# Kernel optimization log

Hardware: AMD Instinct MI355X
Metric: run time of the kernel (lower is better)

## Reference

```python
import jax, jax.numpy as jnp
import numpy as np

N_USER = 50000
N_ITEM = 50000
N_EDGE = 600000
D = 128


def _mean_agg(msg, dst, num_nodes):
    # segment-sum of messages and edge counts; nodes with no in-edges get 0 (DGL semantics)
    s = jax.ops.segment_sum(msg, dst, num_segments=num_nodes)
    cnt = jax.ops.segment_sum(jnp.ones((dst.shape[0], 1), msg.dtype), dst, num_segments=num_nodes)
    return s / jnp.maximum(cnt, 1.0)


def setup_inputs() -> dict:
    key = jax.random.key(0)
    ks = jax.random.split(key, 14)
    scale = 1.0 / np.sqrt(D)
    return {
        "feat_user": jax.random.normal(ks[0], (N_USER, D), jnp.float32),
        "feat_item": jax.random.normal(ks[1], (N_ITEM, D), jnp.float32),
        "W_uu": jax.random.normal(ks[2], (D, D), jnp.float32) * scale,
        "b_uu": jax.random.normal(ks[3], (D,), jnp.float32) * scale,
        "W_ub": jax.random.normal(ks[4], (D, D), jnp.float32) * scale,
        "b_ub": jax.random.normal(ks[5], (D,), jnp.float32) * scale,
        "W_iu": jax.random.normal(ks[6], (D, D), jnp.float32) * scale,
        "b_iu": jax.random.normal(ks[7], (D,), jnp.float32) * scale,
        "src_uu": jax.random.randint(ks[8], (N_EDGE,), 0, N_USER, jnp.int32),
        "dst_uu": jax.random.randint(ks[9], (N_EDGE,), 0, N_USER, jnp.int32),
        "src_ub": jax.random.randint(ks[10], (N_EDGE,), 0, N_USER, jnp.int32),
        "dst_ub": jax.random.randint(ks[11], (N_EDGE,), 0, N_ITEM, jnp.int32),
        "src_iu": jax.random.randint(ks[12], (N_EDGE,), 0, N_ITEM, jnp.int32),
        "dst_iu": jax.random.randint(ks[13], (N_EDGE,), 0, N_USER, jnp.int32),
    }


def reference(feat_user, feat_item, W_uu, b_uu, W_ub, b_ub, W_iu, b_iu,
              src_uu, dst_uu, src_ub, dst_ub, src_iu, dst_iu):
    # per-edge-type linear projection of src node features
    Wh_uu = feat_user @ W_uu + b_uu   # (user, follows, user)
    Wh_ub = feat_user @ W_ub + b_ub   # (user, buys, item)
    Wh_iu = feat_item @ W_iu + b_iu   # (item, bought_by, user)
    # copy_u -> mean per dst node, per edge type
    h_uu = _mean_agg(Wh_uu[src_uu], dst_uu, N_USER)
    h_ub = _mean_agg(Wh_ub[src_ub], dst_ub, N_ITEM)
    h_iu = _mean_agg(Wh_iu[src_iu], dst_iu, N_USER)
    # cross-type combine = 'sum' per dst ntype
    out_user = h_uu + h_iu
    out_item = h_ub
    return out_user, out_item
```

## Files before the change

kernel.cpp:

```cpp
#include <hip/hip_runtime.h>
#include <stdint.h>
#include <string.h>

#define N_USER 50000
#define N_ITEM 50000
#define N_EDGE 600000
#define D 128
#define NTOT 150000
#define ETOT 1800000
#define NB 147
#define BSH 10
#define SPAN 1024
#define CHUNK 4096

typedef unsigned short u16;
typedef unsigned int   u32;
typedef __attribute__((ext_vector_type(8))) short short8;
typedef __attribute__((ext_vector_type(4))) float floatx4;

static __device__ __forceinline__ u16 f2b(float f) {
  u32 x; memcpy(&x, &f, 4);
  u32 r = x + 0x7fffu + ((x >> 16) & 1u);
  return (u16)(r >> 16);
}
static __device__ __forceinline__ float blo2f(u32 v) {
  u32 x = v << 16; float f; memcpy(&f, &x, 4); return f;
}
static __device__ __forceinline__ float bhi2f(u32 v) {
  u32 x = v & 0xffff0000u; float f; memcpy(&f, &x, 4); return f;
}

__global__ void __launch_bounds__(256) k_front(
    const int* __restrict__ duu, const int* __restrict__ dub, const int* __restrict__ diu,
    int* __restrict__ bhist,
    const float* __restrict__ W0, const float* __restrict__ W1, const float* __restrict__ W2,
    u16* __restrict__ WT,
    const float* __restrict__ fu, const float* __restrict__ fi,
    u16* __restrict__ fb_u, u16* __restrict__ fb_i) {
  int bid = blockIdx.x;
  if (bid < 440) {
    __shared__ int h[NB];
    for (int i = threadIdx.x; i < NB; i += 256) h[i] = 0;
    __syncthreads();
    int base = bid * CHUNK;
    for (int j = threadIdx.x; j < CHUNK; j += 256) {
      int e = base + j;
      if (e < ETOT) {
        int t = e / N_EDGE, i = e - t * N_EDGE;
        int d = (t == 0) ? duu[i] : ((t == 1) ? dub[i] : diu[i]);
        atomicAdd(&h[(t * N_USER + d) >> BSH], 1);
      }
    }
    __syncthreads();
    for (int i = threadIdx.x; i < NB; i += 256) if (h[i]) atomicAdd(&bhist[i], h[i]);
  } else if (bid < 443) {
    int wsel = bid - 440;
    for (int idx = threadIdx.x; idx < D * D; idx += 256) {
      int n = idx >> 7, k = idx & 127;
      if (wsel == 0)      WT[n * 256 + k]       = f2b(W0[k * D + n]);
      else if (wsel == 1) WT[n * 256 + 128 + k] = f2b(W2[k * D + n]);
      else                WT[32768 + n * D + k] = f2b(W1[k * D + n]);
    }
  } else {
    int g = bid - 443;
    const float* src = fu; u16* dst = fb_u;
    if (g >= 6250) { g -= 6250; src = fi; dst = fb_i; }
    int gid = g * 256 + threadIdx.x;
    float4 v = ((const float4*)src)[gid];
    union { u16 u[4]; uint2 d; } pk;
    pk.u[0] = f2b(v.x); pk.u[1] = f2b(v.y); pk.u[2] = f2b(v.z); pk.u[3] = f2b(v.w);
    ((uint2*)dst)[gid] = pk.d;
  }
}

__global__ void __launch_bounds__(256) k_bplace(
    const int* __restrict__ suu, const int* __restrict__ duu,
    const int* __restrict__ sub, const int* __restrict__ dub,
    const int* __restrict__ siu, const int* __restrict__ diu,
    const int* __restrict__ bhist, int* __restrict__ cursor,
    int* __restrict__ boff, u32* __restrict__ ebuf) {
  __shared__ int h[NB];
  __shared__ int sboff[NB];
  __shared__ int buf[256];
  int t = threadIdx.x;
  int v = (t < NB) ? bhist[t] : 0;
  buf[t] = v; __syncthreads();
  for (int s = 1; s < 256; s <<= 1) {
    int y = (t >= s) ? buf[t - s] : 0;
    __syncthreads(); buf[t] += y; __syncthreads();
  }
  if (t < NB) sboff[t] = (t == 0) ? 0 : buf[t - 1];
  if (blockIdx.x == 0 && t <= NB) boff[t] = (t == 0) ? 0 : buf[t - 1];
  for (int i = t; i < NB; i += 256) h[i] = 0;
  __syncthreads();
  int base = blockIdx.x * CHUNK;
  u32 pay[16], br[16];
#pragma unroll
  for (int k = 0; k < 16; ++k) {
    int e = base + k * 256 + t;
    br[k] = 0xFFFFFFFFu;
    if (e < ETOT) {
      int ty = e / N_EDGE, i = e - ty * N_EDGE;
      int d, s;
      if (ty == 0)      { d = duu[i]; s = suu[i]; }
      else if (ty == 1) { d = dub[i]; s = sub[i]; }
      else              { d = diu[i]; s = siu[i]; }
      int slot = ty * N_USER + d;
      int bu = slot >> BSH;
      int rank = atomicAdd(&h[bu], 1);
      pay[k] = (u32)s | ((u32)(slot & (SPAN - 1)) << 16);
      br[k]  = (u32)bu | ((u32)rank << 8);
    }
  }
  __syncthreads();
  for (int i = t; i < NB; i += 256)
    h[i] = sboff[i] + atomicAdd(&cursor[i], h[i]);
  __syncthreads();
#pragma unroll
  for (int k = 0; k < 16; ++k) {
    if (br[k] != 0xFFFFFFFFu) {
      int bu = br[k] & 0xFF, rank = (int)(br[k] >> 8);
      ebuf[h[bu] + rank] = pay[k];
    }
  }
}

__global__ void __launch_bounds__(256) k_csr(const int* __restrict__ boff, const u32* __restrict__ ebuf,
                                             int* __restrict__ off, u16* __restrict__ ssrc) {
  __shared__ int sc[SPAN];
  __shared__ int so[SPAN];
  __shared__ int part[256];
  int b = blockIdx.x;
  int ebase = boff[b], ecnt = boff[b + 1] - ebase;
  int sbase = b << BSH;
  int nslots = (NTOT - sbase < SPAN) ? (NTOT - sbase) : SPAN;
  for (int i = threadIdx.x; i < SPAN; i += 256) sc[i] = 0;
  __syncthreads();
  for (int j = threadIdx.x; j < ecnt; j += 256)
    atomicAdd(&sc[ebuf[ebase + j] >> 16], 1);
  __syncthreads();
  int t = threadIdx.x;
  int s0 = sc[4*t], s1 = sc[4*t+1], s2 = sc[4*t+2], s3 = sc[4*t+3];
  int tsum = s0 + s1 + s2 + s3;
  part[t] = tsum; __syncthreads();
  for (int s = 1; s < 256; s <<= 1) {
    int y = (t >= s) ? part[t - s] : 0;
    __syncthreads(); part[t] += y; __syncthreads();
  }
  int pbase = part[t] - tsum;
  so[4*t]   = pbase;
  so[4*t+1] = pbase + s0;
  so[4*t+2] = pbase + s0 + s1;
  so[4*t+3] = pbase + s0 + s1 + s2;
  __syncthreads();
  for (int i = threadIdx.x; i < nslots; i += 256)
    off[sbase + i] = ebase + so[i];
  if (b == 0 && threadIdx.x == 0) off[NTOT] = ETOT;
  for (int i = threadIdx.x; i < SPAN; i += 256) sc[i] = so[i];
  __syncthreads();
  for (int j = threadIdx.x; j < ecnt; j += 256) {
    u32 p = ebuf[ebase + j];
    int pos = atomicAdd(&sc[p >> 16], 1);
    ssrc[ebase + pos] = (u16)(p & 0xFFFFu);
  }
}

__global__ void __launch_bounds__(256) k_mean(const u16* __restrict__ fb_u, const u16* __restrict__ fb_i,
                                              const int* __restrict__ off, const u16* __restrict__ ssrc,
                                              u16* __restrict__ ob) {
  int slot = blockIdx.x * 8 + (threadIdx.x >> 5);
  int lane = threadIdx.x & 31;
  if (slot >= NTOT) return;
  int t = slot / N_USER;
  int d = slot - t * N_USER;
  const u16* fb = (t == 2) ? fb_i : fb_u;
  int s = off[slot], e = off[slot + 1];
  int n = e - s;
  int my_src = (lane < n) ? (int)ssrc[s + lane] : 0;
  float a0 = 0.f, a1 = 0.f, a2 = 0.f, a3 = 0.f;
  int m = (n < 32) ? n : 32;
  int i = 0;
  for (; i + 4 <= m; i += 4) {
    int s0 = __shfl(my_src, i, 32);
    int s1 = __shfl(my_src, i + 1, 32);
    int s2 = __shfl(my_src, i + 2, 32);
    int s3 = __shfl(my_src, i + 3, 32);
    uint2 v0 = ((const uint2*)(fb + (size_t)s0 * D))[lane];
    uint2 v1 = ((const uint2*)(fb + (size_t)s1 * D))[lane];
    uint2 v2 = ((const uint2*)(fb + (size_t)s2 * D))[lane];
    uint2 v3 = ((const uint2*)(fb + (size_t)s3 * D))[lane];
    a0 += blo2f(v0.x) + blo2f(v1.x) + blo2f(v2.x) + blo2f(v3.x);
    a1 += bhi2f(v0.x) + bhi2f(v1.x) + bhi2f(v2.x) + bhi2f(v3.x);
    a2 += blo2f(v0.y) + blo2f(v1.y) + blo2f(v2.y) + blo2f(v3.y);
    a3 += bhi2f(v0.y) + bhi2f(v1.y) + bhi2f(v2.y) + bhi2f(v3.y);
  }
  for (; i < m; ++i) {
    int sr = __shfl(my_src, i, 32);
    uint2 v = ((const uint2*)(fb + (size_t)sr * D))[lane];
    a0 += blo2f(v.x); a1 += bhi2f(v.x);
    a2 += blo2f(v.y); a3 += bhi2f(v.y);
  }
  for (int j = s + 32; j < e; ++j) {
    int sr = ssrc[j];
    uint2 v = ((const uint2*)(fb + (size_t)sr * D))[lane];
    a0 += blo2f(v.x); a1 += bhi2f(v.x);
    a2 += blo2f(v.y); a3 += bhi2f(v.y);
  }
  float inv = (n > 0) ? 1.0f / (float)n : 0.f;
  u32 p0 = (u32)f2b(a0 * inv) | ((u32)f2b(a1 * inv) << 16);
  u32 p1 = (u32)f2b(a2 * inv) | ((u32)f2b(a3 * inv) << 16);
  u32* mrow;
  if (t == 0)      mrow = (u32*)(ob + (size_t)d * 256);
  else if (t == 2) mrow = (u32*)(ob + (size_t)d * 256 + 128);
  else             mrow = (u32*)(ob + 12800000 + (size_t)d * 256);
  ((uint2*)mrow)[lane] = make_uint2(p0, p1);
}

__global__ void __launch_bounds__(256, 2) k_out(float* out, const u16* __restrict__ WT,
                                                const float* __restrict__ buu, const float* __restrict__ bub,
                                                const float* __restrict__ biu, const int* __restrict__ off) {
  int users = (blockIdx.y == 0);
  int tid = threadIdx.x;
  int w = tid >> 6, lane = tid & 63, quad = lane >> 4, l16 = lane & 15;
  int KT = users ? 8 : 4;
  const u16* Wsrc = users ? WT : (WT + 32768);
  int wstride = users ? 256 : 128;

  __shared__ u16 sB[32768];
  int nfrag = KT * 8 * 64;
  for (int fid = tid; fid < nfrag; fid += 256) {
    int fl = fid & 63, fnt = (fid >> 6) & 7, fkk = fid >> 9;
    int fq = fl >> 4, fl16 = fl & 15;
    const u16* src = Wsrc + (fnt * 16 + fl16) * wstride + fkk * 32 + fq * 8;
    *(uint4*)(sB + (size_t)fid * 8) = *(const uint4*)src;
  }
  __syncthreads();

  int row0 = blockIdx.x * 128 + w * 32;
  const u16* ob = (const u16*)out;
  const u16* Abase = users ? ob : (ob + 12800000);
  size_t outoff = users ? 0 : (size_t)N_USER;

  int r0a = row0 + l16, r1a = row0 + 16 + l16;
  int rA0 = r0a < N_USER ? r0a : N_USER - 1;
  int rA1 = r1a < N_USER ? r1a : N_USER - 1;
  const u16* A0 = Abase + (size_t)rA0 * 256 + quad * 8;
  const u16* A1 = Abase + (size_t)rA1 * 256 + quad * 8;

  floatx4 acc[2][8];
#pragma unroll
  for (int rt = 0; rt < 2; ++rt)
#pragma unroll
    for (int nt = 0; nt < 8; ++nt) acc[rt][nt] = (floatx4){0.f, 0.f, 0.f, 0.f};

  for (int kk = 0; kk < KT; ++kk) {
    short8 af0 = *(const short8*)(A0 + kk * 32);
    short8 af1 = *(const short8*)(A1 + kk * 32);
    const short8* bp = (const short8*)(sB + ((size_t)kk * 8 * 64 + lane) * 8);
#pragma unroll
    for (int nt = 0; nt < 8; ++nt) {
      short8 bf = bp[nt * 64];
      acc[0][nt] = __builtin_amdgcn_mfma_f32_16x16x32_bf16(af0, bf, acc[0][nt], 0, 0, 0);
      acc[1][nt] = __builtin_amdgcn_mfma_f32_16x16x32_bf16(af1, bf, acc[1][nt], 0, 0, 0);
    }
  }

#pragma unroll
  for (int rt = 0; rt < 2; ++rt) {
    int tbase = row0 + rt * 16;
    int nA[4], nB[4];
#pragma unroll
    for (int i = 0; i < 4; ++i) {
      int grow = tbase + quad * 4 + i;
      bool ok = grow < N_USER;
      if (users) {
        nA[i] = ok ? (off[grow + 1] - off[grow]) : 0;
        nB[i] = ok ? (off[2 * N_USER + grow + 1] - off[2 * N_USER + grow]) : 0;
      } else {
        nA[i] = ok ? (off[N_USER + grow + 1] - off[N_USER + grow]) : 0;
        nB[i] = 0;
      }
    }
#pragma unroll
    for (int nt = 0; nt < 8; ++nt) {
      int col = nt * 16 + l16;
      float bA = users ? buu[col] : bub[col];
      float bB = users ? biu[col] : 0.f;
#pragma unroll
      for (int i = 0; i < 4; ++i) {
        int grow = tbase + quad * 4 + i;
        if (grow < N_USER) {
          float r = acc[rt][nt][i] + (nA[i] > 0 ? bA : 0.f) + (nB[i] > 0 ? bB : 0.f);
          out[(outoff + (size_t)grow) * D + col] = r;
        }
      }
    }
  }
}

extern "C" void kernel_launch(void* const* d_in, const int* in_sizes, int n_in,
                              void* d_out, int out_size, void* d_ws, size_t ws_size,
                              hipStream_t stream) {
  const float* fu  = (const float*)d_in[0];
  const float* fi  = (const float*)d_in[1];
  const float* Wuu = (const float*)d_in[2];
  const float* buu = (const float*)d_in[3];
  const float* Wub = (const float*)d_in[4];
  const float* bub = (const float*)d_in[5];
  const float* Wiu = (const float*)d_in[6];
  const float* biu = (const float*)d_in[7];
  const int* suu = (const int*)d_in[8];
  const int* duu = (const int*)d_in[9];
  const int* sub = (const int*)d_in[10];
  const int* dub = (const int*)d_in[11];
  const int* siu = (const int*)d_in[12];
  const int* diu = (const int*)d_in[13];
  float* out = (float*)d_out;
  u16* ob = (u16*)d_out;

  int* wsi    = (int*)d_ws;
  int* off    = wsi;
  int* bhist  = wsi + 150016;
  int* cursor = wsi + 150208;
  int* boff   = wsi + 150400;
  u32* ebuf   = (u32*)(wsi + 150592);
  u16* ssrc   = (u16*)(wsi + 1950592);
  u16* WT     = (u16*)(wsi + 2850592);
  u16* fb_u   = (u16*)(wsi + 2875168);
  u16* fb_i   = (u16*)(wsi + 6075168);

  hipMemsetAsync(bhist, 0, 384 * sizeof(int), stream);
  k_front<<<443 + 12500, 256, 0, stream>>>(duu, dub, diu, bhist, Wuu, Wub, Wiu, WT,
                                           fu, fi, fb_u, fb_i);
  k_bplace<<<440, 256, 0, stream>>>(suu, duu, sub, dub, siu, diu, bhist, cursor, boff, ebuf);
  k_csr<<<NB, 256, 0, stream>>>(boff, ebuf, off, ssrc);
  k_mean<<<18750, 256, 0, stream>>>(fb_u, fb_i, off, ssrc, ob);
  k_out<<<dim3(391, 2), 256, 0, stream>>>(out, WT, buu, bub, biu, off);
}
```

Measured before the change: 286.4 us.

## Halve CSR bucket span, batch bf16 conversion per block, prefetch GEMM operands

The destination bucket size drops from 1024 to 512 slots, doubling the bucket count so the CSR-building kernel runs more blocks with less work each. The scans and rank packing are adjusted to handle two buckets per thread and 9-bit bucket ids. The feature-to-bf16 conversion now does eight float4 per thread in fewer blocks instead of one each. In the output GEMM, all A fragments and the degree counts are loaded before the shared-memory barrier so global latency overlaps the weight staging, at the cost of more registers.

New measurement: 279.9 us. -2.3%, faster.

```diff
diff --git a/kernel.cpp b/kernel.cpp
--- a/kernel.cpp
+++ b/kernel.cpp
@@ -8,9 +8,9 @@
 #define D 128
 #define NTOT 150000
 #define ETOT 1800000
-#define NB 147
-#define BSH 10
-#define SPAN 1024
+#define NB 293
+#define BSH 9
+#define SPAN 512
 #define CHUNK 4096
 
 typedef unsigned short u16;
@@ -62,14 +62,19 @@
       else                WT[32768 + n * D + k] = f2b(W1[k * D + n]);
     }
   } else {
-    int g = bid - 443;
-    const float* src = fu; u16* dst = fb_u;
-    if (g >= 6250) { g -= 6250; src = fi; dst = fb_i; }
-    int gid = g * 256 + threadIdx.x;
-    float4 v = ((const float4*)src)[gid];
-    union { u16 u[4]; uint2 d; } pk;
-    pk.u[0] = f2b(v.x); pk.u[1] = f2b(v.y); pk.u[2] = f2b(v.z); pk.u[3] = f2b(v.w);
-    ((uint2*)dst)[gid] = pk.d;
+    int base = (bid - 443) * 2048;
+#pragma unroll
+    for (int u = 0; u < 8; ++u) {
+      int gid = base + u * 256 + threadIdx.x;
+      if (gid < 3200000) {
+        const float* src = fu; u16* dst = fb_u; int g = gid;
+        if (g >= 1600000) { g -= 1600000; src = fi; dst = fb_i; }
+        float4 v = ((const float4*)src)[g];
+        union { u16 u[4]; uint2 d; } pk;
+        pk.u[0] = f2b(v.x); pk.u[1] = f2b(v.y); pk.u[2] = f2b(v.z); pk.u[3] = f2b(v.w);
+        ((uint2*)dst)[g] = pk.d;
+      }
+    }
   }
 }
 
@@ -83,14 +88,21 @@
   __shared__ int sboff[NB];
   __shared__ int buf[256];
   int t = threadIdx.x;
-  int v = (t < NB) ? bhist[t] : 0;
-  buf[t] = v; __syncthreads();
+  int a = (2 * t < NB) ? bhist[2 * t] : 0;
+  int b = (2 * t + 1 < NB) ? bhist[2 * t + 1] : 0;
+  buf[t] = a + b; __syncthreads();
   for (int s = 1; s < 256; s <<= 1) {
     int y = (t >= s) ? buf[t - s] : 0;
     __syncthreads(); buf[t] += y; __syncthreads();
   }
-  if (t < NB) sboff[t] = (t == 0) ? 0 : buf[t - 1];
-  if (blockIdx.x == 0 && t <= NB) boff[t] = (t == 0) ? 0 : buf[t - 1];
+  int ex = buf[t] - (a + b);
+  if (2 * t < NB) sboff[2 * t] = ex;
+  if (2 * t + 1 < NB) sboff[2 * t + 1] = ex + a;
+  if (blockIdx.x == 0) {
+    if (2 * t < NB) boff[2 * t] = ex;
+    if (2 * t + 1 < NB) boff[2 * t + 1] = ex + a;
+    if (t == 255) boff[NB] = buf[255];
+  }
   for (int i = t; i < NB; i += 256) h[i] = 0;
   __syncthreads();
   int base = blockIdx.x * CHUNK;
@@ -109,7 +121,7 @@
       int bu = slot >> BSH;
       int rank = atomicAdd(&h[bu], 1);
       pay[k] = (u32)s | ((u32)(slot & (SPAN - 1)) << 16);
-      br[k]  = (u32)bu | ((u32)rank << 8);
+      br[k]  = (u32)bu | ((u32)rank << 9);
     }
   }
   __syncthreads();
@@ -119,7 +131,7 @@
 #pragma unroll
   for (int k = 0; k < 16; ++k) {
     if (br[k] != 0xFFFFFFFFu) {
-      int bu = br[k] & 0xFF, rank = (int)(br[k] >> 8);
+      int bu = br[k] & 0x1FF, rank = (int)(br[k] >> 9);
       ebuf[h[bu] + rank] = pay[k];
     }
   }
@@ -140,18 +152,16 @@
     atomicAdd(&sc[ebuf[ebase + j] >> 16], 1);
   __syncthreads();
   int t = threadIdx.x;
-  int s0 = sc[4*t], s1 = sc[4*t+1], s2 = sc[4*t+2], s3 = sc[4*t+3];
-  int tsum = s0 + s1 + s2 + s3;
+  int s0 = sc[2 * t], s1 = sc[2 * t + 1];
+  int tsum = s0 + s1;
   part[t] = tsum; __syncthreads();
   for (int s = 1; s < 256; s <<= 1) {
     int y = (t >= s) ? part[t - s] : 0;
     __syncthreads(); part[t] += y; __syncthreads();
   }
   int pbase = part[t] - tsum;
-  so[4*t]   = pbase;
-  so[4*t+1] = pbase + s0;
-  so[4*t+2] = pbase + s0 + s1;
-  so[4*t+3] = pbase + s0 + s1 + s2;
+  so[2 * t]     = pbase;
+  so[2 * t + 1] = pbase + s0;
   __syncthreads();
   for (int i = threadIdx.x; i < nslots; i += 256)
     off[sbase + i] = ebase + so[i];
@@ -234,7 +244,6 @@
     const u16* src = Wsrc + (fnt * 16 + fl16) * wstride + fkk * 32 + fq * 8;
     *(uint4*)(sB + (size_t)fid * 8) = *(const uint4*)src;
   }
-  __syncthreads();
 
   int row0 = blockIdx.x * 128 + w * 32;
   const u16* ob = (const u16*)out;
@@ -247,40 +256,53 @@
   const u16* A0 = Abase + (size_t)rA0 * 256 + quad * 8;
   const u16* A1 = Abase + (size_t)rA1 * 256 + quad * 8;
 
+  short8 af0[8], af1[8];
+#pragma unroll
+  for (int kk = 0; kk < 8; ++kk) {
+    if (kk < KT) {
+      af0[kk] = *(const short8*)(A0 + kk * 32);
+      af1[kk] = *(const short8*)(A1 + kk * 32);
+    }
+  }
+  int nA[2][4], nB[2][4];
+#pragma unroll
+  for (int rt = 0; rt < 2; ++rt)
+#pragma unroll
+    for (int i = 0; i < 4; ++i) {
+      int grow = row0 + rt * 16 + quad * 4 + i;
+      bool ok = grow < N_USER;
+      if (users) {
+        nA[rt][i] = ok ? (off[grow + 1] - off[grow]) : 0;
+        nB[rt][i] = ok ? (off[2 * N_USER + grow + 1] - off[2 * N_USER + grow]) : 0;
+      } else {
+        nA[rt][i] = ok ? (off[N_USER + grow + 1] - off[N_USER + grow]) : 0;
+        nB[rt][i] = 0;
+      }
+    }
+  __syncthreads();
+
   floatx4 acc[2][8];
 #pragma unroll
   for (int rt = 0; rt < 2; ++rt)
 #pragma unroll
     for (int nt = 0; nt < 8; ++nt) acc[rt][nt] = (floatx4){0.f, 0.f, 0.f, 0.f};
 
-  for (int kk = 0; kk < KT; ++kk) {
-    short8 af0 = *(const short8*)(A0 + kk * 32);
-    short8 af1 = *(const short8*)(A1 + kk * 32);
-    const short8* bp = (const short8*)(sB + ((size_t)kk * 8 * 64 + lane) * 8);
-#pragma unroll
-    for (int nt = 0; nt < 8; ++nt) {
-      short8 bf = bp[nt * 64];
-      acc[0][nt] = __builtin_amdgcn_mfma_f32_16x16x32_bf16(af0, bf, acc[0][nt], 0, 0, 0);
-      acc[1][nt] = __builtin_amdgcn_mfma_f32_16x16x32_bf16(af1, bf, acc[1][nt], 0, 0, 0);
+#pragma unroll
+  for (int kk = 0; kk < 8; ++kk) {
+    if (kk < KT) {
+      const short8* bp = (const short8*)(sB + ((size_t)kk * 512 + lane) * 8);
+#pragma unroll
+      for (int nt = 0; nt < 8; ++nt) {
+        short8 bf = bp[nt * 64];
+        acc[0][nt] = __builtin_amdgcn_mfma_f32_16x16x32_bf16(af0[kk], bf, acc[0][nt], 0, 0, 0);
+        acc[1][nt] = __builtin_amdgcn_mfma_f32_16x16x32_bf16(af1[kk], bf, acc[1][nt], 0, 0, 0);
+      }
     }
   }
 
 #pragma unroll
   for (int rt = 0; rt < 2; ++rt) {
     int tbase = row0 + rt * 16;
-    int nA[4], nB[4];
-#pragma unroll
-    for (int i = 0; i < 4; ++i) {
-      int grow = tbase + quad * 4 + i;
-      bool ok = grow < N_USER;
-      if (users) {
-        nA[i] = ok ? (off[grow + 1] - off[grow]) : 0;
-        nB[i] = ok ? (off[2 * N_USER + grow + 1] - off[2 * N_USER + grow]) : 0;
-      } else {
-        nA[i] = ok ? (off[N_USER + grow + 1] - off[N_USER + grow]) : 0;
-        nB[i] = 0;
-      }
-    }
 #pragma unroll
     for (int nt = 0; nt < 8; ++nt) {
       int col = nt * 16 + l16;
@@ -290,7 +312,7 @@
       for (int i = 0; i < 4; ++i) {
         int grow = tbase + quad * 4 + i;
         if (grow < N_USER) {
-          float r = acc[rt][nt][i] + (nA[i] > 0 ? bA : 0.f) + (nB[i] > 0 ? bB : 0.f);
+          float r = acc[rt][nt][i] + (nA[rt][i] > 0 ? bA : 0.f) + (nB[rt][i] > 0 ? bB : 0.f);
           out[(outoff + (size_t)grow) * D + col] = r;
         }
       }
@@ -321,17 +343,17 @@
   int* wsi    = (int*)d_ws;
   int* off    = wsi;
   int* bhist  = wsi + 150016;
-  int* cursor = wsi + 150208;
-  int* boff   = wsi + 150400;
-  u32* ebuf   = (u32*)(wsi + 150592);
-  u16* ssrc   = (u16*)(wsi + 1950592);
-  u16* WT     = (u16*)(wsi + 2850592);
-  u16* fb_u   = (u16*)(wsi + 2875168);
-  u16* fb_i   = (u16*)(wsi + 6075168);
-
-  hipMemsetAsync(bhist, 0, 384 * sizeof(int), stream);
-  k_front<<<443 + 12500, 256, 0, stream>>>(duu, dub, diu, bhist, Wuu, Wub, Wiu, WT,
-                                           fu, fi, fb_u, fb_i);
+  int* cursor = wsi + 150336;
+  int* boff   = wsi + 150656;
+  u32* ebuf   = (u32*)(wsi + 150976);
+  u16* ssrc   = (u16*)(wsi + 1950976);
+  u16* WT     = (u16*)(wsi + 2850976);
+  u16* fb_u   = (u16*)(wsi + 2875552);
+  u16* fb_i   = (u16*)(wsi + 6075552);
+
+  hipMemsetAsync(bhist, 0, 640 * sizeof(int), stream);
+  k_front<<<443 + 1563, 256, 0, stream>>>(duu, dub, diu, bhist, Wuu, Wub, Wiu, WT,
+                                          fu, fi, fb_u, fb_i);
   k_bplace<<<440, 256, 0, stream>>>(suu, duu, sub, dub, siu, diu, bhist, cursor, boff, ebuf);
   k_csr<<<NB, 256, 0, stream>>>(boff, ebuf, off, ssrc);
   k_mean<<<18750, 256, 0, stream>>>(fb_u, fb_i, off, ssrc, ob);
```
